# Optimization experiments

Hardware: AMD Instinct MI355X
Metric: run time of the kernel (lower is better)

The kernel has to match this reference:

```python
import jax, jax.numpy as jnp
import numpy as np
import math

B, S, D, H = 2, 2048, 1024, 16
DH = D // H
NEG = -1e9


def gelu(x):
    return 0.5 * x * (1.0 + jnp.tanh(math.sqrt(2.0 / math.pi) * (x + 0.044715 * x ** 3)))


def layernorm(x, g, b, eps=1e-6):
    # faithful to module: uses std (unbiased, N-1) and adds eps to std, not var
    mean = jnp.mean(x, axis=-1, keepdims=True)
    var = jnp.sum((x - mean) ** 2, axis=-1, keepdims=True) / (x.shape[-1] - 1)
    std = jnp.sqrt(var)
    return g * (x - mean) / (std + eps) + b


def setup_inputs() -> dict:
    key = jax.random.key(0)
    ks = jax.random.split(key, 13)
    sd = 0.02
    return {
        "x": jax.random.normal(ks[0], (B, S, D), jnp.float32),
        "w_attn": jax.random.normal(ks[1], (D, 3 * D), jnp.float32) * sd,
        "b_attn": jnp.zeros((3 * D,), jnp.float32),
        "w_aproj": jax.random.normal(ks[2], (D, D), jnp.float32) * sd,
        "b_aproj": jnp.zeros((D,), jnp.float32),
        "g1": jnp.ones((D,), jnp.float32),
        "b1": jnp.zeros((D,), jnp.float32),
        "w_fc": jax.random.normal(ks[3], (D, 4 * D), jnp.float32) * sd,
        "b_fc": jnp.zeros((4 * D,), jnp.float32),
        "w_mproj": jax.random.normal(ks[4], (4 * D, D), jnp.float32) * sd,
        "b_mproj": jnp.zeros((D,), jnp.float32),
        "g2": jnp.ones((D,), jnp.float32),
        "b2": jnp.zeros((D,), jnp.float32),
    }


def reference(x, w_attn, b_attn, w_aproj, b_aproj, g1, b1, w_fc, b_fc, w_mproj, b_mproj, g2, b2):
    # --- attention ---
    qkv = x @ w_attn + b_attn                       # [B,S,3D]
    q, k, v = jnp.split(qkv, 3, axis=2)
    q = q.reshape(B, S, H, DH).transpose(0, 2, 1, 3)  # [B,H,S,DH]
    k = k.reshape(B, S, H, DH).transpose(0, 2, 1, 3)
    v = v.reshape(B, S, H, DH).transpose(0, 2, 1, 3)
    w = jnp.einsum('bhqd,bhkd->bhqk', q, k) / math.sqrt(DH)
    mask = jnp.tril(jnp.ones((S, S), jnp.float32))[None, None]
    w = w * mask + NEG * (1.0 - mask)
    w = jax.nn.softmax(w, axis=-1)
    a = jnp.einsum('bhqk,bhkd->bhqd', w, v)         # [B,H,S,DH]
    a = a.transpose(0, 2, 1, 3).reshape(B, S, D)
    a = a @ w_aproj + b_aproj
    # --- postLN + MLP ---
    n = layernorm(x + a, g1, b1)
    h = gelu(n @ w_fc + b_fc)
    m = h @ w_mproj + b_mproj
    return layernorm(n + m, g2, b2)
```

## Files before the change

### kernel.cpp

```cpp
#include <hip/hip_runtime.h>
#include <type_traits>


typedef unsigned short u16;
typedef short s16x8 __attribute__((ext_vector_type(8)));
typedef unsigned short u16x4 __attribute__((ext_vector_type(4)));
typedef float f32x4 __attribute__((ext_vector_type(4)));
typedef float f32x16 __attribute__((ext_vector_type(16)));

__device__ __forceinline__ u16 f2b(float f) {
    union { float f; unsigned u; } x{f};
    unsigned r = x.u + 0x7FFFu + ((x.u >> 16) & 1u);
    return (u16)(r >> 16);
}

__device__ __forceinline__ float b2f(u16 v) {
    union { unsigned u; float f; } x;
    x.u = ((unsigned)v) << 16;
    return x.f;
}

__device__ __forceinline__ f32x4 mfma16(s16x8 a, s16x8 b, f32x4 c) {
    return __builtin_amdgcn_mfma_f32_16x16x32_bf16(a, b, c, 0, 0, 0);
}

__device__ __forceinline__ f32x16 mfma32(s16x8 a, s16x8 b, f32x16 c) {
    return __builtin_amdgcn_mfma_f32_32x32x16_bf16(a, b, c, 0, 0, 0);
}

__device__ __forceinline__ int cvtpk(float a, float b) {
    int r;
    asm("v_cvt_pk_bf16_f32 %0, %1, %2" : "=v"(r) : "v"(a), "v"(b));
    return r;
}

__device__ __forceinline__ void gld_lds16(const u16* g, const u16* l) {
    __builtin_amdgcn_global_load_lds(
        (const __attribute__((address_space(1))) void*)g,
        (__attribute__((address_space(3))) void*)l, 16, 0, 0);
}

__device__ __forceinline__ void hard_barrier() {
    __builtin_amdgcn_sched_barrier(0);
    __builtin_amdgcn_s_barrier();
    __builtin_amdgcn_sched_barrier(0);
}

__global__ __launch_bounds__(256) void cvt_bf16(const float* __restrict__ in,
                                                u16* __restrict__ out, int n4) {
    int i = blockIdx.x * 256 + threadIdx.x;
    if (i < n4) {
        float4 v = ((const float4*)in)[i];
        u16x4 o = {f2b(v.x), f2b(v.y), f2b(v.z), f2b(v.w)};
        ((u16x4*)out)[i] = o;
    }
}

__global__ __launch_bounds__(256) void transpose_bf16(const float* __restrict__ W,
                                                      u16* __restrict__ WT,
                                                      int K, int N) {
    __shared__ float t[32][33];
    int tx = threadIdx.x & 31, ty = threadIdx.x >> 5;
    int n0 = blockIdx.x * 32, k0 = blockIdx.y * 32;
    #pragma unroll
    for (int r = ty; r < 32; r += 8)
        t[r][tx] = W[(size_t)(k0 + r) * N + n0 + tx];
    __syncthreads();
    #pragma unroll
    for (int r = ty; r < 32; r += 8)
        WT[(size_t)(n0 + r) * K + k0 + tx] = f2b(t[tx][r]);
}

template<int BN, bool GELU, typename OT, bool VW = false, bool C2D = false>
__global__ __launch_bounds__(512) void gemm_pl(const u16* __restrict__ A,
                                               const u16* __restrict__ BT,
                                               const float* __restrict__ bias,
                                               OT* __restrict__ C,
                                               u16* __restrict__ vTout,
                                               int M, int N, int K, int ldc) {
    constexpr int NF = BN / 64;
    constexpr int BNI = BN / 64;
    constexpr int LTOT = 2 + BNI;
    __shared__ u16 As[2][128 * 64];
    __shared__ u16 Bs[2][BN * 64];

    int t = threadIdx.x;
    int w = t >> 6, l = t & 63, l16 = l & 15, lh = l >> 4;
    int wr = w >> 2, wc = w & 3;

    int nbm = M >> 7;
    int id = blockIdx.x;
    size_t m0, n0;
    if constexpr (C2D) {
        int x = id & 7, j = id >> 3;
        int ntn2 = (int)(gridDim.x >> 6);
        int mi = (x & 3) * 8 + (j & 7);
        int ni = (x >> 2) * ntn2 + (j >> 3);
        m0 = (size_t)mi * 128;
        n0 = (size_t)ni * BN;
    } else {
        int cpx = gridDim.x >> 3;
        int id2 = (id & 7) * cpx + (id >> 3);
        m0 = (size_t)(id2 % nbm) * 128;
        n0 = (size_t)(id2 / nbm) * BN;
    }

    int rowA = t >> 3;
    int gc2 = (t & 7) ^ (rowA & 7);
    const u16* Ag = A + (m0 + rowA) * (size_t)K + gc2 * 8;
    const u16* Bg = BT + (n0 + rowA) * (size_t)K + gc2 * 8;
    int wb = w * 512;

    f32x4 acc[4][NF] = {};
    int rx = (l16 & 7) * 8;

    #pragma unroll
    for (int j = 0; j < 2; ++j)
        gld_lds16(Ag + (size_t)j * 64 * K, &As[0][j * 4096 + wb]);
    #pragma unroll
    for (int j = 0; j < BNI; ++j)
        gld_lds16(Bg + (size_t)j * 64 * K, &Bs[0][j * 4096 + wb]);
    #pragma unroll
    for (int j = 0; j < 2; ++j)
        gld_lds16(Ag + 64 + (size_t)j * 64 * K, &As[1][j * 4096 + wb]);
    #pragma unroll
    for (int j = 0; j < BNI; ++j)
        gld_lds16(Bg + 64 + (size_t)j * 64 * K, &Bs[1][j * 4096 + wb]);

#define GTILE(CB, kk, LAST)                                                   \
    {                                                                         \
        if (LAST) asm volatile("s_waitcnt vmcnt(0)" ::: "memory");            \
        else      asm volatile("s_waitcnt vmcnt(%0)" :: "n"(LTOT) : "memory");\
        hard_barrier();                                                       \
        __builtin_amdgcn_s_setprio(1);                                        \
        _Pragma("unroll")                                                     \
        for (int ks = 0; ks < 2; ++ks) {                                      \
            s16x8 af[4], bf[NF];                                              \
            _Pragma("unroll")                                                 \
            for (int fm = 0; fm < 4; ++fm) {                                  \
                int row = wr * 64 + fm * 16 + l16;                            \
                int col = ((ks * 4 + lh) * 8) ^ rx;                           \
                af[fm] = *(const s16x8*)&As[CB][row * 64 + col];              \
            }                                                                 \
            _Pragma("unroll")                                                 \
            for (int fn = 0; fn < NF; ++fn) {                                 \
                int row = wc * (BN / 4) + fn * 16 + l16;                      \
                int col = ((ks * 4 + lh) * 8) ^ rx;                           \
                bf[fn] = *(const s16x8*)&Bs[CB][row * 64 + col];              \
            }                                                                 \
            _Pragma("unroll")                                                 \
            for (int fm = 0; fm < 4; ++fm)                                    \
                _Pragma("unroll")                                             \
                for (int fn = 0; fn < NF; ++fn)                               \
                    acc[fm][fn] = mfma16(af[fm], bf[fn], acc[fm][fn]);        \
        }                                                                     \
        __builtin_amdgcn_s_setprio(0);                                        \
        hard_barrier();                                                       \
        if ((kk) + 128 < K) {                                                 \
            const u16* Ap = Ag + (kk) + 128;                                  \
            _Pragma("unroll")                                                 \
            for (int j = 0; j < 2; ++j)                                       \
                gld_lds16(Ap + (size_t)j * 64 * K, &As[CB][j * 4096 + wb]);   \
            const u16* Bp = Bg + (kk) + 128;                                  \
            _Pragma("unroll")                                                 \
            for (int j = 0; j < BNI; ++j)                                     \
                gld_lds16(Bp + (size_t)j * 64 * K, &Bs[CB][j * 4096 + wb]);   \
        }                                                                     \
    }

    for (int k0 = 0; k0 < K; k0 += 128) {
        GTILE(0, k0, (k0 + 64 >= K))
        GTILE(1, k0 + 64, (k0 + 128 >= K))
    }
#undef GTILE

    #pragma unroll
    for (int fn = 0; fn < NF; ++fn) {
        size_t col = n0 + wc * (BN / 4) + fn * 16 + l16;
        float bs = bias[col];
        #pragma unroll
        for (int fm = 0; fm < 4; ++fm) {
            size_t row0 = m0 + wr * 64 + fm * 16 + lh * 4;
            u16x4 pack;
            #pragma unroll
            for (int i = 0; i < 4; ++i) {
                float v = acc[fm][fn][i] + bs;
                if constexpr (GELU) {
                    float x3 = v * v * v;
                    v = 0.5f * v * (1.f + tanhf(0.7978845608f * (v + 0.044715f * x3)));
                }
                if constexpr (std::is_same<OT, u16>::value) {
                    u16 q = f2b(v);
                    C[(row0 + i) * ldc + col] = q;
                    pack[i] = q;
                } else {
                    C[(row0 + i) * ldc + col] = v;
                }
            }
            if constexpr (VW) {
                if (n0 >= 2048) {
                    int hh = ((int)col - 2048) >> 6;
                    int dd = ((int)col - 2048) & 63;
                    size_t vrow = (size_t)(((row0 >> 11) * 16 + hh) * 64 + dd);
                    *(u16x4*)(vTout + vrow * 2048 + (row0 & 2047)) = pack;
                }
            }
        }
    }
}

template<bool GELU, typename OT>
__global__ __launch_bounds__(512) void gemm_pl3(const u16* __restrict__ A,
                                                const u16* __restrict__ BT,
                                                const float* __restrict__ bias,
                                                OT* __restrict__ C,
                                                int M, int N, int K, int ldc) {
    __shared__ u16 As[3][128 * 64];
    __shared__ u16 Bs[3][64 * 64];

    int t = threadIdx.x;
    int w = t >> 6, l = t & 63, l16 = l & 15, lh = l >> 4;
    int wr = w >> 2, wc = w & 3;

    int id = blockIdx.x;
    int x = id & 7, j = id >> 3;
    int mi = (x & 3) * 8 + (j & 7);
    int ni = (x >> 2) * 8 + (j >> 3);
    size_t m0 = (size_t)mi * 128;
    size_t n0 = (size_t)ni * 64;

    int rowA = t >> 3;
    int gc2 = (t & 7) ^ (rowA & 7);
    const u16* Ag = A + (m0 + rowA) * (size_t)K + gc2 * 8;
    const u16* Bg = BT + (n0 + rowA) * (size_t)K + gc2 * 8;
    int wb = w * 512;

    f32x4 acc[4] = {};
    int rx = (l16 & 7) * 8;

#define STAGE3(KK, BUF)                                                       \
    {                                                                         \
        gld_lds16(Ag + (KK), &As[BUF][wb]);                                   \
        gld_lds16(Ag + (KK) + (size_t)64 * K, &As[BUF][4096 + wb]);           \
        gld_lds16(Bg + (KK), &Bs[BUF][wb]);                                   \
    }

    int NT = K >> 6;
    STAGE3(0, 0)
    STAGE3(64, 1)
    if (NT > 2) STAGE3(128, 2)

    int cur = 0;
    #pragma unroll 1
    for (int kt = 0; kt < NT; ++kt) {
        if (kt + 2 < NT)      asm volatile("s_waitcnt vmcnt(6)" ::: "memory");
        else if (kt + 1 < NT) asm volatile("s_waitcnt vmcnt(3)" ::: "memory");
        else                  asm volatile("s_waitcnt vmcnt(0)" ::: "memory");
        hard_barrier();

        __builtin_amdgcn_s_setprio(1);
        #pragma unroll
        for (int ks = 0; ks < 2; ++ks) {
            s16x8 af[4], bf;
            #pragma unroll
            for (int fm = 0; fm < 4; ++fm) {
                int row = wr * 64 + fm * 16 + l16;
                int col = ((ks * 4 + lh) * 8) ^ rx;
                af[fm] = *(const s16x8*)&As[cur][row * 64 + col];
            }
            {
                int row = wc * 16 + l16;
                int col = ((ks * 4 + lh) * 8) ^ rx;
                bf = *(const s16x8*)&Bs[cur][row * 64 + col];
            }
            #pragma unroll
            for (int fm = 0; fm < 4; ++fm)
                acc[fm] = mfma16(af[fm], bf, acc[fm]);
        }
        __builtin_amdgcn_s_setprio(0);
        hard_barrier();

        if (kt + 3 < NT) STAGE3((size_t)(kt + 3) * 64, cur)
        cur = (cur == 2) ? 0 : cur + 1;
    }
#undef STAGE3

    size_t col = n0 + wc * 16 + l16;
    float bs = bias[col];
    #pragma unroll
    for (int fm = 0; fm < 4; ++fm) {
        size_t row0 = m0 + wr * 64 + fm * 16 + lh * 4;
        #pragma unroll
        for (int i = 0; i < 4; ++i) {
            float v = acc[fm][i] + bs;
            if constexpr (GELU) {
                float x3 = v * v * v;
                v = 0.5f * v * (1.f + tanhf(0.7978845608f * (v + 0.044715f * x3)));
            }
            if constexpr (std::is_same<OT, u16>::value)
                C[(row0 + i) * ldc + col] = f2b(v);
            else
                C[(row0 + i) * ldc + col] = v;
        }
    }
}

__global__ __launch_bounds__(256) void attn_kernel(const u16* __restrict__ qkv,
                                                   const u16* __restrict__ vT,
                                                   u16* __restrict__ p0,
                                                   u16* __restrict__ p1,
                                                   u16* __restrict__ p2,
                                                   u16* __restrict__ p3,
                                                   float2* __restrict__ stats) {
    constexpr int S = 2048, D3 = 3072, Dm = 1024;
    __shared__ u16 Kl[2][64 * 64];
    __shared__ u16 Vt[2][64 * 64];

    int t = threadIdx.x;
    int w = t >> 6, l = t & 63;
    int l32 = l & 31, hi = l >> 5;
    int bid = blockIdx.x;
    int bh = (bid & 7) * 4 + ((bid >> 3) & 3);
    int rest = bid >> 5;
    int quar = rest & 3;
    int pr = rest >> 2;
    int b = bh >> 4, h = bh & 15;
    size_t base = (size_t)b * S * D3;

    u16* pout = quar == 0 ? p0 : (quar == 1 ? p1 : (quar == 2 ? p2 : p3));

    int rK0 = t >> 3, gK = t & 7;
    int rK1 = rK0 + 32;
    size_t koff0 = (size_t)rK0 * D3 + (size_t)((gK ^ (rK0 & 7)) * 8);
    size_t koff1 = (size_t)rK1 * D3 + (size_t)((gK ^ (rK1 & 7)) * 8);
    const u16* kbase = qkv + base + Dm + h * 64;
    size_t voff0 = (size_t)(bh * 64 + rK0) * 2048 + (size_t)((gK ^ (rK0 & 7)) * 8);
    size_t voff1 = (size_t)(bh * 64 + 32 + rK0) * 2048 + (size_t)((gK ^ (rK0 & 7)) * 8);

    constexpr float cexp = 0.18033688011112042f;
    constexpr float THR = 64.0f;
    int xg = l32 & 7;

#define STAGE(SC, BUF)                                                        \
    {                                                                         \
        size_t ko_ = (size_t)(SC) * 64 * D3;                                  \
        int kvb_ = (SC) * 64;                                                 \
        gld_lds16(kbase + ko_ + koff0, &Kl[BUF][w * 512]);                    \
        gld_lds16(kbase + ko_ + koff1, &Kl[BUF][2048 + w * 512]);             \
        gld_lds16(vT + voff0 + kvb_, &Vt[BUF][w * 512]);                      \
        gld_lds16(vT + voff1 + kvb_, &Vt[BUF][2048 + w * 512]);               \
    }

    #pragma unroll 1
    for (int ph = 0; ph < 2; ++ph) {
        int qt = ph ? (15 - pr) : pr;
        int qb = qt * 128 + w * 32;
        int nst = 2 * (qt + 1);
        int c0 = (nst * quar) >> 2;
        int c1 = (nst * (quar + 1)) >> 2;

        f32x16 O0 = {}, O1 = {};
        float m = -1e30f, lr = 0.f;

        if (c0 < c1) {
            s16x8 qf[4];
            const u16* qp = qkv + base + (size_t)(qb + l32) * D3 + h * 64 + hi * 8;
            #pragma unroll
            for (int kk = 0; kk < 4; ++kk)
                qf[kk] = *(const s16x8*)(qp + kk * 16);

            STAGE(c0, 0)
            if (c0 + 1 < c1) STAGE(c0 + 1, 1)

            int cur = 0;
            #pragma unroll 1
            for (int sc = c0; sc < c1; ++sc) {
                if (sc + 1 < c1)
                    asm volatile("s_waitcnt vmcnt(4)" ::: "memory");
                else
                    asm volatile("s_waitcnt vmcnt(0)" ::: "memory");
                hard_barrier();

                int kvb = sc * 64;
                int navail = ((qb - kvb) >> 5) + 1;
                if (navail > 0) {
                    if (navail > 2) navail = 2;
                    const u16* Kc = Kl[cur];
                    const u16* Vc = Vt[cur];
                    f32x16 sa0 = {}, sa1 = {};
                    #pragma unroll
                    for (int kk = 0; kk < 4; ++kk) {
                        s16x8 kf = *(const s16x8*)&Kc[l32 * 64 + (((2 * kk + hi) ^ xg) * 8)];
                        sa0 = mfma32(kf, qf[kk], sa0);
                    }
                    if (navail == 2) {
                        #pragma unroll
                        for (int kk = 0; kk < 4; ++kk) {
                            s16x8 kf = *(const s16x8*)&Kc[(32 + l32) * 64 + (((2 * kk + hi) ^ xg) * 8)];
                            sa1 = mfma32(kf, qf[kk], sa1);
                        }
                    }
                    bool diag0 = (kvb == qb);
                    bool diag1 = (kvb + 32 == qb);
                    float p[32];
                    float mx = -1e30f;
                    if (diag0 | diag1) {
                        #pragma unroll
                        for (int reg = 0; reg < 16; ++reg) {
                            int kvloc = (reg & 3) + 8 * (reg >> 2) + 4 * hi;
                            float s0 = sa0[reg];
                            if (diag0 && kvloc > l32) s0 = -1e30f;
                            p[reg] = s0;
                            mx = fmaxf(mx, s0);
                        }
                        if (navail == 2) {
                            #pragma unroll
                            for (int reg = 0; reg < 16; ++reg) {
                                int kvloc = (reg & 3) + 8 * (reg >> 2) + 4 * hi;
                                float s1 = sa1[reg];
                                if (diag1 && kvloc > l32) s1 = -1e30f;
                                p[16 + reg] = s1;
                                mx = fmaxf(mx, s1);
                            }
                        }
                    } else {
                        #pragma unroll
                        for (int reg = 0; reg < 16; ++reg) {
                            p[reg] = sa0[reg];
                            mx = fmaxf(mx, sa0[reg]);
                        }
                        if (navail == 2) {
                            #pragma unroll
                            for (int reg = 0; reg < 16; ++reg) {
                                p[16 + reg] = sa1[reg];
                                mx = fmaxf(mx, sa1[reg]);
                            }
                        }
                    }
                    mx = fmaxf(mx, __shfl_xor(mx, 32));
                    if (!__all(mx <= m + THR)) {
                        float mn = fmaxf(m, mx);
                        float a_ = exp2f(cexp * (m - mn));
                        m = mn;
                        #pragma unroll
                        for (int reg = 0; reg < 16; ++reg) {
                            int src = (reg & 3) + 8 * (reg >> 2) + 4 * hi;
                            float aq = __shfl(a_, src);
                            O0[reg] *= aq;
                            O1[reg] *= aq;
                        }
                        lr *= a_;
                    }
                    float cm = cexp * m;
                    float rs = 0.f;
                    #pragma unroll
                    for (int reg = 0; reg < 16; ++reg) {
                        p[reg] = exp2f(fmaf(cexp, p[reg], -cm));
                        rs += p[reg];
                    }
                    if (navail == 2) {
                        #pragma unroll
                        for (int reg = 16; reg < 32; ++reg) {
                            p[reg] = exp2f(fmaf(cexp, p[reg], -cm));
                            rs += p[reg];
                        }
                    }
                    rs += __shfl_xor(rs, 32);
                    lr += rs;

                    #pragma unroll
                    for (int c = 0; c < 4; ++c) {
                        if (c < navail * 2) {
                            int pb = (c >> 1) * 16 + (c & 1) * 8;
                            int pk01 = cvtpk(p[pb + 0], p[pb + 1]);
                            int pk23 = cvtpk(p[pb + 2], p[pb + 3]);
                            int pk45 = cvtpk(p[pb + 4], p[pb + 5]);
                            int pk67 = cvtpk(p[pb + 6], p[pb + 7]);
                            int sx01 = __shfl_xor(pk01, 32);
                            int sx23 = __shfl_xor(pk23, 32);
                            int sx45 = __shfl_xor(pk45, 32);
                            int sx67 = __shfl_xor(pk67, 32);
                            union { int i[4]; s16x8 v; } u;
                            u.i[0] = hi ? sx45 : pk01;
                            u.i[1] = hi ? sx67 : pk23;
                            u.i[2] = hi ? pk45 : sx01;
                            u.i[3] = hi ? pk67 : sx23;
                            int go = ((c * 2 + hi) ^ xg) * 8;
                            s16x8 vb0 = *(const s16x8*)&Vc[l32 * 64 + go];
                            O0 = mfma32(u.v, vb0, O0);
                            s16x8 vb1 = *(const s16x8*)&Vc[(32 + l32) * 64 + go];
                            O1 = mfma32(u.v, vb1, O1);
                        }
                    }
                }

                hard_barrier();
                if (sc + 2 < c1) STAGE(sc + 2, cur)
                cur ^= 1;
            }
        }

        size_t obase = (size_t)b * S * 1024 + h * 64;
        #pragma unroll
        for (int reg = 0; reg < 16; ++reg) {
            int src = (reg & 3) + 8 * (reg >> 2) + 4 * hi;
            size_t row = obase + (size_t)(qb + src) * 1024;
            pout[row + l32] = f2b(O0[reg]);
            pout[row + 32 + l32] = f2b(O1[reg]);
        }
        if (hi == 0) {
            float2 st; st.x = m; st.y = lr;
            stats[quar * 65536 + ((b * 2048 + qb + l32) * 16 + h)] = st;
        }
    }
#undef STAGE
}

__global__ __launch_bounds__(256) void merge_attn(u16* __restrict__ p0,
                                                  const u16* __restrict__ p1,
                                                  const u16* __restrict__ p2,
                                                  const u16* __restrict__ p3,
                                                  const float2* __restrict__ stats) {
    constexpr float cexp = 0.18033688011112042f;
    int gid = blockIdx.x * 256 + threadIdx.x;
    int rh = gid >> 2;
    int dc = (gid & 3) * 16;
    int R = rh >> 4, h = rh & 15;
    size_t addr = (size_t)R * 1024 + h * 64 + dc;

    float2 s0 = stats[rh];
    float2 s1 = stats[65536 + rh];
    float2 s2 = stats[131072 + rh];
    float2 s3 = stats[196608 + rh];
    float M = fmaxf(fmaxf(s0.x, s1.x), fmaxf(s2.x, s3.x));
    float a0 = exp2f(cexp * (s0.x - M));
    float a1 = exp2f(cexp * (s1.x - M));
    float a2 = exp2f(cexp * (s2.x - M));
    float a3 = exp2f(cexp * (s3.x - M));
    float inv = 1.f / (a0 * s0.y + a1 * s1.y + a2 * s2.y + a3 * s3.y);
    a0 *= inv; a1 *= inv; a2 *= inv; a3 *= inv;

    u16x4 o[4];
    #pragma unroll
    for (int j = 0; j < 4; ++j) {
        u16x4 q0 = *(const u16x4*)(p0 + addr + j * 4);
        u16x4 q1 = *(const u16x4*)(p1 + addr + j * 4);
        u16x4 q2 = *(const u16x4*)(p2 + addr + j * 4);
        u16x4 q3 = *(const u16x4*)(p3 + addr + j * 4);
        #pragma unroll
        for (int e = 0; e < 4; ++e)
            o[j][e] = f2b(a0 * b2f(q0[e]) + a1 * b2f(q1[e]) +
                          a2 * b2f(q2[e]) + a3 * b2f(q3[e]));
    }
    #pragma unroll
    for (int j = 0; j < 4; ++j)
        *(u16x4*)(p0 + addr + j * 4) = o[j];
}

template<bool WB>
__global__ __launch_bounds__(256) void resln(const float* __restrict__ xa,
                                             const float* __restrict__ xb2,
                                             const float* __restrict__ g,
                                             const float* __restrict__ be,
                                             float* __restrict__ outf,
                                             u16* __restrict__ outb) {
    int row = blockIdx.x;
    int t = threadIdx.x;
    size_t base = (size_t)row * 1024 + t * 4;
    float4 va = *(const float4*)(xa + base);
    float4 vb = *(const float4*)(xb2 + base);
    float v0 = va.x + vb.x, v1 = va.y + vb.y, v2 = va.z + vb.z, v3 = va.w + vb.w;
    float s1 = v0 + v1 + v2 + v3;
    float s2 = v0 * v0 + v1 * v1 + v2 * v2 + v3 * v3;
    #pragma unroll
    for (int off = 32; off >= 1; off >>= 1) {
        s1 += __shfl_down(s1, off);
        s2 += __shfl_down(s2, off);
    }
    __shared__ float r1[4], r2[4];
    if ((t & 63) == 0) { r1[t >> 6] = s1; r2[t >> 6] = s2; }
    __syncthreads();
    s1 = r1[0] + r1[1] + r1[2] + r1[3];
    s2 = r2[0] + r2[1] + r2[2] + r2[3];
    float mean = s1 * (1.f / 1024.f);
    float var = fmaxf((s2 - 1024.f * mean * mean) * (1.f / 1023.f), 0.f);
    float inv = 1.f / (sqrtf(var) + 1e-6f);
    int col = t * 4;
    float y0 = g[col + 0] * ((v0 - mean) * inv) + be[col + 0];
    float y1 = g[col + 1] * ((v1 - mean) * inv) + be[col + 1];
    float y2 = g[col + 2] * ((v2 - mean) * inv) + be[col + 2];
    float y3 = g[col + 3] * ((v3 - mean) * inv) + be[col + 3];
    float4 o = {y0, y1, y2, y3};
    *(float4*)(outf + base) = o;
    if constexpr (WB) {
        u16x4 ob = {f2b(y0), f2b(y1), f2b(y2), f2b(y3)};
        *(u16x4*)(outb + base) = ob;
    }
}

extern "C" void kernel_launch(void* const* d_in, const int* in_sizes, int n_in,
                              void* d_out, int out_size, void* d_ws, size_t ws_size,
                              hipStream_t stream) {
    (void)in_sizes; (void)n_in; (void)out_size; (void)ws_size;
    const float* x       = (const float*)d_in[0];
    const float* w_attn  = (const float*)d_in[1];
    const float* b_attn  = (const float*)d_in[2];
    const float* w_aproj = (const float*)d_in[3];
    const float* b_aproj = (const float*)d_in[4];
    const float* g1      = (const float*)d_in[5];
    const float* b1      = (const float*)d_in[6];
    const float* w_fc    = (const float*)d_in[7];
    const float* b_fc    = (const float*)d_in[8];
    const float* w_mproj = (const float*)d_in[9];
    const float* b_mproj = (const float*)d_in[10];
    const float* g2      = (const float*)d_in[11];
    const float* b2      = (const float*)d_in[12];
    float* out = (float*)d_out;

    constexpr int M = 4096;
    constexpr int D = 1024;

    char* ws = (char*)d_ws;
    u16*   slotA = (u16*)ws;
    char*  pB    = ws + (32u << 20);
    char*  pC    = ws + (40u << 20);
    char*  pD    = ws + (48u << 20);
    char*  pE    = ws + (64u << 20);

    u16*   xb    = (u16*)pB;
    u16*   wT    = (u16*)pC;
    u16*   qkv   = slotA;
    u16*   vT    = slotA + (24u << 20) / 2;
    u16*   part0 = (u16*)pB;
    u16*   part1 = (u16*)pC;
    u16*   part2 = (u16*)pD;
    u16*   part3 = (u16*)(pD + (8u << 20));
    float2* stat = (float2*)pE;
    u16*   abuf  = (u16*)pB;
    float* aout  = (float*)pD;
    float* nbuf  = (float*)pE;
    u16*   nb    = (u16*)pB;
    u16*   h     = slotA;
    float* mout  = (float*)pD;

    dim3 blk(256);
    dim3 blk512(512);

    cvt_bf16<<<dim3(4096), blk, 0, stream>>>(x, xb, M * D / 4);

    transpose_bf16<<<dim3(3072 / 32, 1024 / 32), blk, 0, stream>>>(w_attn, wT, 1024, 3072);
    gemm_pl<128, false, u16, true><<<dim3((M / 128) * (3072 / 128)), blk512, 0, stream>>>(
        xb, wT, b_attn, qkv, vT, M, 3072, 1024, 3072);

    attn_kernel<<<dim3(1024), blk, 0, stream>>>(qkv, vT, part0, part1, part2, part3, stat);
    merge_attn<<<dim3(1024), blk, 0, stream>>>(part0, part1, part2, part3, stat);

    transpose_bf16<<<dim3(1024 / 32, 1024 / 32), blk, 0, stream>>>(w_aproj, wT, 1024, 1024);
    gemm_pl3<false, float><<<dim3((M / 128) * (1024 / 64)), blk512, 0, stream>>>(
        abuf, wT, b_aproj, aout, M, 1024, 1024, 1024);

    resln<true><<<dim3(M), blk, 0, stream>>>(x, aout, g1, b1, nbuf, nb);

    transpose_bf16<<<dim3(4096 / 32, 1024 / 32), blk, 0, stream>>>(w_fc, wT, 1024, 4096);
    gemm_pl<128, true, u16, false, true><<<dim3((M / 128) * (4096 / 128)), blk512, 0, stream>>>(
        nb, wT, b_fc, h, nullptr, M, 4096, 1024, 4096);

    transpose_bf16<<<dim3(1024 / 32, 4096 / 32), blk, 0, stream>>>(w_mproj, wT, 4096, 1024);
    gemm_pl3<false, float><<<dim3((M / 128) * (1024 / 64)), blk512, 0, stream>>>(
        h, wT, b_mproj, mout, M, 1024, 4096, 1024);

    resln<false><<<dim3(M), blk, 0, stream>>>(nbuf, mout, g2, b2, out, nullptr);
}
```

Measured before the change: 265.7 us.

## Use 256x256 tile GEMM kernel for the MLP fc projection with GELU

Adds a new bf16 MFMA GEMM kernel with 256x256 output tiles, double-buffered async global-to-LDS loads and a swizzled LDS layout, and uses it for the fc GEMM with fused bias and GELU. The larger tile raises arithmetic intensity per loaded byte and cuts redundant A/B traffic. The block-index mapping groups tiles for L2 locality. In exchange it uses 128KB of LDS per block and many accumulator registers, which limits occupancy to one block per CU, and it launches only 256 blocks. It also stores output as scalar 16-bit values rather than vector writes.

```diff
diff --git a/kernel.cpp b/kernel.cpp
--- a/kernel.cpp
+++ b/kernel.cpp
@@ -69,6 +69,117 @@
     #pragma unroll
     for (int r = ty; r < 32; r += 8)
         WT[(size_t)(n0 + r) * K + k0 + tx] = f2b(t[tx][r]);
+}
+
+template<bool GELU, typename OT>
+__global__ __launch_bounds__(512) void gemm256(const u16* __restrict__ A,
+                                               const u16* __restrict__ BT,
+                                               const float* __restrict__ bias,
+                                               OT* __restrict__ C,
+                                               int M, int N, int K, int ldc) {
+    __shared__ u16 As[2][256 * 64];
+    __shared__ u16 Bs[2][256 * 64];
+
+    int t = threadIdx.x;
+    int w = t >> 6, l = t & 63, l16 = l & 15, lh = l >> 4;
+    int wr = w >> 2, wc = w & 3;
+
+    int id = blockIdx.x;
+    int x = id & 7, j = id >> 3;
+    int ntn2 = (int)(gridDim.x >> 5);
+    int mi = (x & 3) * 4 + (j & 3);
+    int ni = (x >> 2) * ntn2 + (j >> 2);
+    size_t m0 = (size_t)mi * 256;
+    size_t n0 = (size_t)ni * 256;
+
+    int rowA = t >> 3;
+    int gc2 = (t & 7) ^ (rowA & 7);
+    const u16* Ag = A + (m0 + rowA) * (size_t)K + gc2 * 8;
+    const u16* Bg = BT + (n0 + rowA) * (size_t)K + gc2 * 8;
+    int t8 = t * 8;
+
+    f32x4 acc[8][4] = {};
+    int rx = l16 & 7;
+
+#define ST256(KK, BUF)                                                       \
+    {                                                                        \
+        _Pragma("unroll")                                                    \
+        for (int jj = 0; jj < 4; ++jj)                                       \
+            gld_lds16(Ag + (KK) + (size_t)(jj * 64) * K,                     \
+                      &As[BUF][jj * 4096 + t8]);                             \
+        _Pragma("unroll")                                                    \
+        for (int jj = 0; jj < 4; ++jj)                                       \
+            gld_lds16(Bg + (KK) + (size_t)(jj * 64) * K,                     \
+                      &Bs[BUF][jj * 4096 + t8]);                             \
+    }
+
+    int NT = K >> 6;
+    ST256(0, 0)
+    ST256(64, 1)
+
+    #pragma unroll 1
+    for (int kt = 0; kt < NT; ++kt) {
+        if (kt + 1 < NT) asm volatile("s_waitcnt vmcnt(8)" ::: "memory");
+        else             asm volatile("s_waitcnt vmcnt(0)" ::: "memory");
+        hard_barrier();
+
+        int cur = kt & 1;
+        s16x8 af[8][2], bf[4][2];
+        #pragma unroll
+        for (int fm = 0; fm < 8; ++fm)
+            #pragma unroll
+            for (int ks = 0; ks < 2; ++ks) {
+                int row = wr * 128 + fm * 16 + l16;
+                int col = (((ks * 4 + lh) ^ rx) * 8);
+                af[fm][ks] = *(const s16x8*)&As[cur][row * 64 + col];
+            }
+        #pragma unroll
+        for (int fn = 0; fn < 4; ++fn)
+            #pragma unroll
+            for (int ks = 0; ks < 2; ++ks) {
+                int row = wc * 64 + fn * 16 + l16;
+                int col = (((ks * 4 + lh) ^ rx) * 8);
+                bf[fn][ks] = *(const s16x8*)&Bs[cur][row * 64 + col];
+            }
+        asm volatile("s_waitcnt lgkmcnt(0)" ::: "memory");
+        __builtin_amdgcn_sched_barrier(0);
+        hard_barrier();
+
+        if (kt + 2 < NT) ST256((size_t)(kt + 2) * 64, cur)
+
+        __builtin_amdgcn_s_setprio(1);
+        #pragma unroll
+        for (int fm = 0; fm < 8; ++fm)
+            #pragma unroll
+            for (int fn = 0; fn < 4; ++fn) {
+                acc[fm][fn] = mfma16(af[fm][0], bf[fn][0], acc[fm][fn]);
+                acc[fm][fn] = mfma16(af[fm][1], bf[fn][1], acc[fm][fn]);
+            }
+        __builtin_amdgcn_s_setprio(0);
+    }
+#undef ST256
+
+    #pragma unroll
+    for (int fn = 0; fn < 4; ++fn) {
+        size_t col = n0 + wc * 64 + fn * 16 + l16;
+        float bs = bias[col];
+        #pragma unroll
+        for (int fm = 0; fm < 8; ++fm) {
+            size_t row0 = m0 + wr * 128 + fm * 16 + lh * 4;
+            #pragma unroll
+            for (int i = 0; i < 4; ++i) {
+                float v = acc[fm][fn][i] + bs;
+                if constexpr (GELU) {
+                    float x3 = v * v * v;
+                    v = 0.5f * v * (1.f + tanhf(0.7978845608f * (v + 0.044715f * x3)));
+                }
+                if constexpr (std::is_same<OT, u16>::value)
+                    C[(row0 + i) * ldc + col] = f2b(v);
+                else
+                    C[(row0 + i) * ldc + col] = v;
+            }
+        }
+    }
 }
 
 template<int BN, bool GELU, typename OT, bool VW = false, bool C2D = false>
@@ -662,8 +773,8 @@
     resln<true><<<dim3(M), blk, 0, stream>>>(x, aout, g1, b1, nbuf, nb);
 
     transpose_bf16<<<dim3(4096 / 32, 1024 / 32), blk, 0, stream>>>(w_fc, wT, 1024, 4096);
-    gemm_pl<128, true, u16, false, true><<<dim3((M / 128) * (4096 / 128)), blk512, 0, stream>>>(
-        nb, wT, b_fc, h, nullptr, M, 4096, 1024, 4096);
+    gemm256<true, u16><<<dim3((M / 256) * (4096 / 256)), blk512, 0, stream>>>(
+        nb, wT, b_fc, h, M, 4096, 1024, 4096);
 
     transpose_bf16<<<dim3(1024 / 32, 4096 / 32), blk, 0, stream>>>(w_mproj, wT, 4096, 1024);
     gemm_pl3<false, float><<<dim3((M / 128) * (1024 / 64)), blk512, 0, stream>>>(
```

Result: no change. 268.0 us (+0.9%).
